# Kernel optimization log

Measured on AMD Instinct MI355X. Metric: run time of the kernel, lower is better.

Reference implementation:

```python
import jax, jax.numpy as jnp
import numpy as np
from jax import lax

B, D, T = 16, 256, 8192
N_CB, CB_SIZE, CB_DIM = 7, 1024, 8
EPS = 1e-12


def setup_inputs() -> dict:
    key = jax.random.key(0)
    ks = jax.random.split(key, 9)
    z = jax.random.normal(ks[0], (B, D, T), dtype=jnp.float32)
    # weight-normalized 1x1 conv params (v direction, g magnitude, bias)
    in_v = jax.random.normal(ks[1], (N_CB, CB_DIM, D), dtype=jnp.float32) * 0.05
    in_g = jax.random.uniform(ks[2], (N_CB, CB_DIM), minval=0.5, maxval=1.5, dtype=jnp.float32)
    in_b = jax.random.normal(ks[3], (N_CB, CB_DIM), dtype=jnp.float32) * 0.01
    out_v = jax.random.normal(ks[4], (N_CB, D, CB_DIM), dtype=jnp.float32) * 0.05
    out_g = jax.random.uniform(ks[5], (N_CB, D), minval=0.5, maxval=1.5, dtype=jnp.float32)
    out_b = jax.random.normal(ks[6], (N_CB, D), dtype=jnp.float32) * 0.01
    codebooks = jax.random.normal(ks[7], (N_CB, CB_SIZE, CB_DIM), dtype=jnp.float32)
    return {"z": z, "in_v": in_v, "in_g": in_g, "in_b": in_b,
            "out_v": out_v, "out_g": out_g, "out_b": out_b,
            "codebooks": codebooks, "n_quantizers": 7}


def _wn(v, g):
    # torch weight_norm dim=0: per-output-channel direction * magnitude
    return g[:, None] * v / jnp.linalg.norm(v, axis=1, keepdims=True)


def _l2norm(x):
    return x / jnp.maximum(jnp.linalg.norm(x, axis=-1, keepdims=True), EPS)


def reference(z, in_v, in_g, in_b, out_v, out_g, out_b, codebooks, n_quantizers):
    b = z.shape[0]
    residual = z
    z_q = jnp.zeros_like(z)
    commitment_loss = jnp.float32(0.0)
    codebook_loss = jnp.float32(0.0)
    all_indices = []
    for i in range(N_CB):
        w_in = _wn(in_v[i], in_g[i])            # [cd, D]
        z_e = jnp.einsum('cd,bdt->bct', w_in, residual) + in_b[i][None, :, None]  # [B, cd, T]
        enc = z_e.transpose(0, 2, 1).reshape(-1, CB_DIM)        # [(B T), cd]
        enc_n = _l2norm(enc)
        cb_n = _l2norm(codebooks[i])                             # [K, cd]
        dist = (jnp.sum(enc_n**2, axis=1, keepdims=True)
                - 2.0 * enc_n @ cb_n.T
                + jnp.sum(cb_n**2, axis=1)[None, :])             # [(B T), K]
        idx = jnp.argmin(dist, axis=1).reshape(b, -1)            # [B, T]
        z_q_c = codebooks[i][idx].transpose(0, 2, 1)             # [B, cd, T]
        commit_i = jnp.mean((z_e - lax.stop_gradient(z_q_c))**2, axis=(1, 2))  # [B]
        cbl_i = jnp.mean((z_q_c - lax.stop_gradient(z_e))**2, axis=(1, 2))     # [B]
        z_q_ste = z_e + lax.stop_gradient(z_q_c - z_e)
        w_out = _wn(out_v[i], out_g[i])          # [D, cd]
        z_q_i = jnp.einsum('dc,bct->bdt', w_out, z_q_ste) + out_b[i][None, :, None]
        mask = (jnp.full((b,), i) < n_quantizers).astype(z.dtype)  # [B]
        z_q = z_q + z_q_i * mask[:, None, None]
        residual = residual - z_q_i
        commitment_loss = commitment_loss + jnp.mean(commit_i * mask)
        codebook_loss = codebook_loss + jnp.mean(cbl_i * mask)
        all_indices.append(idx)
    return z_q, commitment_loss, codebook_loss, jnp.stack(all_indices, axis=1)
```

## Files before the change

### kernel.cpp

```cpp
#include <hip/hip_runtime.h>
#include <math.h>

#define NCB 7
#define CBK 1024
#define CD  8
#define BB  16
#define DD  256
#define TT  8192
#define BT  (BB*TT)

typedef float v2f __attribute__((ext_vector_type(2)));
typedef float v4f __attribute__((ext_vector_type(4)));

static constexpr size_t ZQN  = (size_t)BB * DD * TT;
static constexpr size_t IDX0 = ZQN + 2;

#define WS_WTINT  16
#define WS_WTOUTT 16400
#define WS_OBT    32784
#define WS_APK    34832
#define WS_UVEC   37968
#define WS_CBP    38032

__global__ void rvq_prep1(const float* __restrict__ in_v, const float* __restrict__ in_g,
                          const float* __restrict__ out_v, const float* __restrict__ out_g,
                          const float* __restrict__ out_b, const float* __restrict__ cb,
                          float* __restrict__ ws, double* __restrict__ lossAcc)
{
#pragma clang fp contract(off)
  int gid = blockIdx.x * blockDim.x + threadIdx.x;
  if (gid == 0) *lossAcc = 0.0;
  if (gid < NCB*DD*CD) {
    int i = gid / (DD*CD); int rem = gid % (DD*CD); int d = rem / CD; int c = rem % CD;
    const float* vrow = in_v + ((size_t)i*CD + c) * DD;
    double acc = 0.0;
    for (int q = 0; q < DD; ++q) { double v = vrow[q]; acc += v*v; }
    float nf = (float)sqrt(acc);
    ws[WS_WTINT + d*64 + i*8 + c] = (in_g[i*CD + c] * vrow[d]) / nf;
  } else if (gid < 2*NCB*DD*CD) {
    int e = gid - NCB*DD*CD;
    int i = e / (DD*CD); int rem = e % (DD*CD); int d = rem / CD; int c = rem % CD;
    const float* vrow = out_v + ((size_t)i*DD + d)*CD;
    double acc = 0.0;
    for (int q = 0; q < CD; ++q) { double v = vrow[q]; acc += v*v; }
    float nf = (float)sqrt(acc);
    ws[WS_WTOUTT + d*64 + i*8 + c] = (out_g[i*DD + d] * vrow[c]) / nf;
  } else if (gid < 2*NCB*DD*CD + DD*8) {
    int e = gid - 2*NCB*DD*CD;
    int d = e >> 3, i = e & 7;
    ws[WS_OBT + d*8 + i] = (i < NCB) ? out_b[i*DD + d] : 0.f;
  } else if (gid < 2*NCB*DD*CD + DD*8 + NCB*CBK) {
    int e = gid - 2*NCB*DD*CD - DD*8;
    int i = e / CBK; int k = e % CBK;
    const float* row = cb + ((size_t)i*CBK + k)*CD;
    double acc = 0.0;
    for (int c = 0; c < CD; ++c) { double v = row[c]; acc += v*v; }
    float nf = fmaxf((float)sqrt(acc), 1e-12f);
    float* rec = ws + WS_CBP + ((size_t)i*512 + (k >> 1))*32;
    int h = k & 1;
    float c2 = 0.f;
    for (int c = 0; c < CD; ++c) {
      float cn = row[c] / nf;
      rec[2*c + h] = cn;
      float s = cn*cn; c2 += s;
    }
    rec[16 + h] = c2;
  }
}

__global__ void rvq_prep2(const float* __restrict__ in_b, const float* __restrict__ out_b,
                          float* __restrict__ ws)
{
#pragma clang fp contract(off)
  int gid = blockIdx.x * blockDim.x + threadIdx.x;
  if (gid < 49*64) {
    int pair = gid / 64; int j = pair / 7; int i2 = pair % 7;
    int e = gid % 64; int cp = e >> 3; int c = e & 7;
    float v = 0.f;
    if (j < i2) {
      double acc = 0.0;
      for (int d = 0; d < DD; ++d)
        acc += (double)ws[WS_WTINT + d*64 + i2*8 + c] * (double)ws[WS_WTOUTT + d*64 + j*8 + cp];
      v = (float)acc;
    }
    ws[WS_APK + pair*64 + cp*8 + c] = v;
  } else if (gid < 49*64 + 64) {
    int e = gid - 49*64; int i = e >> 3; int c = e & 7;
    float v = 0.f;
    if (i < NCB) {
      double s = (double)in_b[i*CD + c];
      for (int j = 0; j < i; ++j)
        for (int d = 0; d < DD; ++d)
          s -= (double)ws[WS_WTINT + d*64 + i*8 + c] * (double)out_b[j*DD + d];
      v = (float)s;
    }
    ws[WS_UVEC + e] = v;
  }
}

__launch_bounds__(256)
__global__ void rvq_quant(const float* __restrict__ z,
                          const float* __restrict__ cb,
                          const int* __restrict__ nqp,
                          const float* __restrict__ ws,
                          float* __restrict__ out, double* __restrict__ lossAcc)
{
#pragma clang fp contract(off)
  const int e = blockIdx.x * 256 + threadIdx.x;
  const int b = e >> 13;
  const int t = e & (TT - 1);
  int nqc = *nqp; nqc = nqc < 0 ? 0 : (nqc > NCB ? NCB : nqc);

  const float* WTINT  = ws + WS_WTINT;
  const float* WTOUTT = ws + WS_WTOUTT;
  const float* OBT    = ws + WS_OBT;
  const float* APK    = ws + WS_APK;
  const float* UVEC   = ws + WS_UVEC;
  const float* CBP    = ws + WS_CBP;

  const float* zc0 = z + (size_t)b*DD*TT + t;

  v2f ze2[28];
#pragma unroll
  for (int h = 0; h < 28; ++h) ze2[h] = (v2f){0.f, 0.f};
#pragma unroll 2
  for (int d = 0; d < DD; ++d) {
    float zv = zc0[(size_t)d*TT];
    const v2f* wv = (const v2f*)(WTINT + d*64);
    v2f zb = (v2f){zv, zv};
#pragma unroll
    for (int h = 0; h < 28; ++h)
      ze2[h] = __builtin_elementwise_fma(wv[h], zb, ze2[h]);
  }
  {
    const v2f* uv = (const v2f*)UVEC;
#pragma unroll
    for (int h = 0; h < 28; ++h) ze2[h] = ze2[h] + uv[h];
  }

  double lacc = 0.0;
  v2f zh[NCB][4];

#pragma unroll
  for (int i = 0; i < NCB; ++i) {
    float zef[CD], en[CD];
#pragma unroll
    for (int h = 0; h < 4; ++h) { zef[2*h] = ze2[i*4 + h].x; zef[2*h + 1] = ze2[i*4 + h].y; }
    float ss = 0.f;
#pragma unroll
    for (int c = 0; c < CD; ++c) { float sq = zef[c]*zef[c]; ss += sq; }
    float den = fmaxf(sqrtf(ss), 1e-12f);
    float a2 = 0.f;
#pragma unroll
    for (int c = 0; c < CD; ++c) {
      float en_ = zef[c] / den;
      en[c] = en_;
      float sq = en_*en_; a2 += sq;
    }

    const v2f* crow = (const v2f*)(CBP + (size_t)i*512*32);
    float best = 3.0e38f; int bk = 0;
#pragma unroll 2
    for (int qq = 0; qq < 512; ++qq) {
      const v2f* rw = crow + qq*16;
      v2f m = rw[0] * (v2f){en[0], en[0]};
#pragma unroll
      for (int c = 1; c < CD; ++c)
        m = __builtin_elementwise_fma(rw[c], (v2f){en[c], en[c]}, m);
      v2f dd = __builtin_elementwise_fma((v2f){-2.f, -2.f}, m, (v2f){a2, a2});
      dd = dd + rw[8];
      bool l0 = dd.x < best; best = l0 ? dd.x : best; bk = l0 ? qq*2     : bk;
      bool l1 = dd.y < best; best = l1 ? dd.y : best; bk = l1 ? qq*2 + 1 : bk;
    }

    const float* qrow = cb + ((size_t)i*CBK + bk)*CD;
    v4f qa = ((const v4f*)qrow)[0];
    v4f qb = ((const v4f*)qrow)[1];
    float zcv[CD] = {qa.x, qa.y, qa.z, qa.w, qb.x, qb.y, qb.z, qb.w};
    float zst[CD];
    float sloc = 0.f;
#pragma unroll
    for (int c = 0; c < CD; ++c) {
      float zv = zef[c];
      zst[c] = zv + (zcv[c] - zv);
      float df = zv - zcv[c];
      float sq = df*df; sloc += sq;
    }
    if (i < nqc) lacc += (double)sloc;
    out[IDX0 + ((size_t)b*NCB + i)*TT + t] = (float)bk;
#pragma unroll
    for (int h = 0; h < 4; ++h) zh[i][h] = (v2f){zst[2*h], zst[2*h + 1]};

#pragma unroll
    for (int i2 = i + 1; i2 < NCB; ++i2) {
      const v2f* av = (const v2f*)(APK + (size_t)(i*7 + i2)*64);
      v2f corr[4];
#pragma unroll
      for (int h = 0; h < 4; ++h) corr[h] = av[h] * (v2f){zst[0], zst[0]};
#pragma unroll
      for (int cp = 1; cp < CD; ++cp) {
        v2f zb = (v2f){zst[cp], zst[cp]};
#pragma unroll
        for (int h = 0; h < 4; ++h)
          corr[h] = __builtin_elementwise_fma(av[cp*4 + h], zb, corr[h]);
      }
#pragma unroll
      for (int h = 0; h < 4; ++h) ze2[i2*4 + h] = ze2[i2*4 + h] - corr[h];
    }
  }

  {
    float* zq = out + (size_t)b*DD*TT + t;
#pragma unroll 2
    for (int d = 0; d < DD; ++d) {
      const v2f* wr = (const v2f*)(WTOUTT + d*64);
      const float* obr = OBT + d*8;
      float acc = 0.f;
#pragma unroll
      for (int i = 0; i < NCB; ++i) {
        if (i < nqc) {
          v2f mm = wr[i*4] * zh[i][0];
          mm = __builtin_elementwise_fma(wr[i*4 + 1], zh[i][1], mm);
          mm = __builtin_elementwise_fma(wr[i*4 + 2], zh[i][2], mm);
          mm = __builtin_elementwise_fma(wr[i*4 + 3], zh[i][3], mm);
          float m = mm.x + mm.y;
          acc += (m + obr[i]);
        }
      }
      zq[(size_t)d*TT] = acc;
    }
  }

#pragma unroll
  for (int off = 32; off >= 1; off >>= 1) lacc += __shfl_down(lacc, off, 64);
  if ((threadIdx.x & 63) == 0) atomicAdd(lossAcc, lacc);
}

__global__ void rvq_fin(const double* __restrict__ lossAcc, float* __restrict__ out) {
  float v = (float)(*lossAcc * (1.0 / 1048576.0));
  out[ZQN]     = v;
  out[ZQN + 1] = v;
}

extern "C" void kernel_launch(void* const* d_in, const int* in_sizes, int n_in,
                              void* d_out, int out_size, void* d_ws, size_t ws_size,
                              hipStream_t stream) {
  const float* z     = (const float*)d_in[0];
  const float* in_v  = (const float*)d_in[1];
  const float* in_g  = (const float*)d_in[2];
  const float* in_b  = (const float*)d_in[3];
  const float* out_v = (const float*)d_in[4];
  const float* out_g = (const float*)d_in[5];
  const float* out_b = (const float*)d_in[6];
  const float* cb    = (const float*)d_in[7];
  const int*   nqp   = (const int*)d_in[8];
  float* out = (float*)d_out;

  float*  ws      = (float*)d_ws;
  double* lossAcc = (double*)d_ws;

  int prep1_n = 2*NCB*DD*CD + DD*8 + NCB*CBK;
  rvq_prep1<<<(prep1_n + 255)/256, 256, 0, stream>>>(in_v, in_g, out_v, out_g,
                                                     out_b, cb, ws, lossAcc);
  rvq_prep2<<<13, 256, 0, stream>>>(in_b, out_b, ws);
  rvq_quant<<<BT/256, 256, 0, stream>>>(z, cb, nqp, ws, out, lossAcc);
  rvq_fin<<<1, 1, 0, stream>>>(lossAcc, out);
}
```

Before: 1.055 ms.

## Split each time position across two wavefronts for input projection, codebook search and output

```diff
diff --git a/kernel.cpp b/kernel.cpp
--- a/kernel.cpp
+++ b/kernel.cpp
@@ -106,9 +106,13 @@
                           float* __restrict__ out, double* __restrict__ lossAcc)
 {
 #pragma clang fp contract(off)
-  const int e = blockIdx.x * 256 + threadIdx.x;
-  const int b = e >> 13;
-  const int t = e & (TT - 1);
+  const int tid = threadIdx.x;
+  const int p   = tid & 63;
+  const int h   = __builtin_amdgcn_readfirstlane((tid >> 6) & 1);
+  const int g   = __builtin_amdgcn_readfirstlane(tid >> 7);
+  const int blk = blockIdx.x;
+  const int b   = blk >> 6;
+  const int t   = ((blk & 63) << 7) + g*64 + p;
   int nqc = *nqp; nqc = nqc < 0 ? 0 : (nqc > NCB ? NCB : nqc);
 
   const float* WTINT  = ws + WS_WTINT;
@@ -118,24 +122,54 @@
   const float* UVEC   = ws + WS_UVEC;
   const float* CBP    = ws + WS_CBP;
 
-  const float* zc0 = z + (size_t)b*DD*TT + t;
+  __shared__ v4f   pex[2][14][64];
+  __shared__ float scb[2][2][64];
+  __shared__ int   sck[2][2][64];
 
   v2f ze2[28];
 #pragma unroll
-  for (int h = 0; h < 28; ++h) ze2[h] = (v2f){0.f, 0.f};
+  for (int x = 0; x < 28; ++x) ze2[x] = (v2f){0.f, 0.f};
+  {
+    const float* zc0 = z + (size_t)b*DD*TT + (size_t)(h*128)*TT + t;
 #pragma unroll 2
-  for (int d = 0; d < DD; ++d) {
-    float zv = zc0[(size_t)d*TT];
-    const v2f* wv = (const v2f*)(WTINT + d*64);
-    v2f zb = (v2f){zv, zv};
-#pragma unroll
-    for (int h = 0; h < 28; ++h)
-      ze2[h] = __builtin_elementwise_fma(wv[h], zb, ze2[h]);
+    for (int j = 0; j < 128; ++j) {
+      float zv = zc0[(size_t)j*TT];
+      const v2f* wv = (const v2f*)(WTINT + (h*128 + j)*64);
+      v2f zb = (v2f){zv, zv};
+#pragma unroll
+      for (int x = 0; x < 28; ++x)
+        ze2[x] = __builtin_elementwise_fma(wv[x], zb, ze2[x]);
+    }
+  }
+
+  if (h) {
+#pragma unroll
+    for (int x = 0; x < 14; ++x)
+      pex[g][x][p] = (v4f){ze2[2*x].x, ze2[2*x].y, ze2[2*x+1].x, ze2[2*x+1].y};
+  }
+  __syncthreads();
+  if (!h) {
+#pragma unroll
+    for (int x = 0; x < 14; ++x) {
+      v4f o = pex[g][x][p];
+      ze2[2*x]   = ze2[2*x]   + (v2f){o.x, o.y};
+      ze2[2*x+1] = ze2[2*x+1] + (v2f){o.z, o.w};
+      pex[g][x][p] = (v4f){ze2[2*x].x, ze2[2*x].y, ze2[2*x+1].x, ze2[2*x+1].y};
+    }
+  }
+  __syncthreads();
+  if (h) {
+#pragma unroll
+    for (int x = 0; x < 14; ++x) {
+      v4f o = pex[g][x][p];
+      ze2[2*x]   = (v2f){o.x, o.y};
+      ze2[2*x+1] = (v2f){o.z, o.w};
+    }
   }
   {
     const v2f* uv = (const v2f*)UVEC;
 #pragma unroll
-    for (int h = 0; h < 28; ++h) ze2[h] = ze2[h] + uv[h];
+    for (int x = 0; x < 28; ++x) ze2[x] = ze2[x] + uv[x];
   }
 
   double lacc = 0.0;
@@ -145,7 +179,7 @@
   for (int i = 0; i < NCB; ++i) {
     float zef[CD], en[CD];
 #pragma unroll
-    for (int h = 0; h < 4; ++h) { zef[2*h] = ze2[i*4 + h].x; zef[2*h + 1] = ze2[i*4 + h].y; }
+    for (int x = 0; x < 4; ++x) { zef[2*x] = ze2[i*4 + x].x; zef[2*x + 1] = ze2[i*4 + x].y; }
     float ss = 0.f;
 #pragma unroll
     for (int c = 0; c < CD; ++c) { float sq = zef[c]*zef[c]; ss += sq; }
@@ -158,22 +192,47 @@
       float sq = en_*en_; a2 += sq;
     }
 
-    const v2f* crow = (const v2f*)(CBP + (size_t)i*512*32);
-    float best = 3.0e38f; int bk = 0;
+    v2f enb[CD];
+#pragma unroll
+    for (int c = 0; c < CD; ++c) enb[c] = (v2f){en[c], en[c]};
+    const v2f a2b = (v2f){a2, a2};
+    const v2f n2b = (v2f){-2.f, -2.f};
+    const v2f* crow = (const v2f*)(CBP + ((size_t)i*512 + h*256)*32);
+    float best0 = 3.0e38f, best1 = 3.0e38f; int bk0 = 0, bk1 = 0;
 #pragma unroll 2
-    for (int qq = 0; qq < 512; ++qq) {
-      const v2f* rw = crow + qq*16;
-      v2f m = rw[0] * (v2f){en[0], en[0]};
-#pragma unroll
-      for (int c = 1; c < CD; ++c)
-        m = __builtin_elementwise_fma(rw[c], (v2f){en[c], en[c]}, m);
-      v2f dd = __builtin_elementwise_fma((v2f){-2.f, -2.f}, m, (v2f){a2, a2});
-      dd = dd + rw[8];
-      bool l0 = dd.x < best; best = l0 ? dd.x : best; bk = l0 ? qq*2     : bk;
-      bool l1 = dd.y < best; best = l1 ? dd.y : best; bk = l1 ? qq*2 + 1 : bk;
-    }
-
-    const float* qrow = cb + ((size_t)i*CBK + bk)*CD;
+    for (int qq = 0; qq < 128; ++qq) {
+      const v2f* r0 = crow + qq*16;
+      const v2f* r1 = crow + (128 + qq)*16;
+      v2f m0 = r0[0]*enb[0];
+      v2f m1 = r1[0]*enb[0];
+#pragma unroll
+      for (int c = 1; c < CD; ++c) {
+        m0 = __builtin_elementwise_fma(r0[c], enb[c], m0);
+        m1 = __builtin_elementwise_fma(r1[c], enb[c], m1);
+      }
+      v2f d0 = __builtin_elementwise_fma(n2b, m0, a2b); d0 = d0 + r0[8];
+      v2f d1 = __builtin_elementwise_fma(n2b, m1, a2b); d1 = d1 + r1[8];
+      int kb0 = (h*256 + qq)*2;
+      int kb1 = (h*256 + 128 + qq)*2;
+      bool l;
+      l = d0.x < best0; best0 = l ? d0.x : best0; bk0 = l ? kb0     : bk0;
+      l = d0.y < best0; best0 = l ? d0.y : best0; bk0 = l ? kb0 + 1 : bk0;
+      l = d1.x < best1; best1 = l ? d1.x : best1; bk1 = l ? kb1     : bk1;
+      l = d1.y < best1; best1 = l ? d1.y : best1; bk1 = l ? kb1 + 1 : bk1;
+    }
+    bool ltS = best1 < best0;
+    float bestT = ltS ? best1 : best0;
+    int   bkT   = ltS ? bk1   : bk0;
+
+    scb[g][h][p] = bestT; sck[g][h][p] = bkT;
+    __syncthreads();
+    float bA = scb[g][0][p]; int kA = sck[g][0][p];
+    float bB = scb[g][1][p]; int kB = sck[g][1][p];
+    bool ltH = bB < bA;
+    int k = ltH ? kB : kA;
+    __syncthreads();
+
+    const float* qrow = cb + ((size_t)i*CBK + k)*CD;
     v4f qa = ((const v4f*)qrow)[0];
     v4f qb = ((const v4f*)qrow)[1];
     float zcv[CD] = {qa.x, qa.y, qa.z, qa.w, qb.x, qb.y, qb.z, qb.w};
@@ -186,33 +245,37 @@
       float df = zv - zcv[c];
       float sq = df*df; sloc += sq;
     }
-    if (i < nqc) lacc += (double)sloc;
-    out[IDX0 + ((size_t)b*NCB + i)*TT + t] = (float)bk;
-#pragma unroll
-    for (int h = 0; h < 4; ++h) zh[i][h] = (v2f){zst[2*h], zst[2*h + 1]};
+    if (h == 0) {
+      if (i < nqc) lacc += (double)sloc;
+      out[IDX0 + ((size_t)b*NCB + i)*TT + t] = (float)k;
+    }
+#pragma unroll
+    for (int x = 0; x < 4; ++x) zh[i][x] = (v2f){zst[2*x], zst[2*x + 1]};
 
 #pragma unroll
     for (int i2 = i + 1; i2 < NCB; ++i2) {
       const v2f* av = (const v2f*)(APK + (size_t)(i*7 + i2)*64);
       v2f corr[4];
 #pragma unroll
-      for (int h = 0; h < 4; ++h) corr[h] = av[h] * (v2f){zst[0], zst[0]};
+      for (int x = 0; x < 4; ++x) corr[x] = av[x] * (v2f){zst[0], zst[0]};
 #pragma unroll
       for (int cp = 1; cp < CD; ++cp) {
         v2f zb = (v2f){zst[cp], zst[cp]};
 #pragma unroll
-        for (int h = 0; h < 4; ++h)
-          corr[h] = __builtin_elementwise_fma(av[cp*4 + h], zb, corr[h]);
+        for (int x = 0; x < 4; ++x)
+          corr[x] = __builtin_elementwise_fma(av[cp*4 + x], zb, corr[x]);
       }
 #pragma unroll
-      for (int h = 0; h < 4; ++h) ze2[i2*4 + h] = ze2[i2*4 + h] - corr[h];
+      for (int x = 0; x < 4; ++x) ze2[i2*4 + x] = ze2[i2*4 + x] - corr[x];
     }
   }
 
   {
     float* zq = out + (size_t)b*DD*TT + t;
+    const int dbase = h*128;
 #pragma unroll 2
-    for (int d = 0; d < DD; ++d) {
+    for (int j = 0; j < 128; ++j) {
+      const int d = dbase + j;
       const v2f* wr = (const v2f*)(WTOUTT + d*64);
       const float* obr = OBT + d*8;
       float acc = 0.f;
@@ -231,9 +294,11 @@
     }
   }
 
-#pragma unroll
-  for (int off = 32; off >= 1; off >>= 1) lacc += __shfl_down(lacc, off, 64);
-  if ((threadIdx.x & 63) == 0) atomicAdd(lossAcc, lacc);
+  if (h == 0) {
+#pragma unroll
+    for (int off = 32; off >= 1; off >>= 1) lacc += __shfl_down(lacc, off, 64);
+    if (p == 0) atomicAdd(lossAcc, lacc);
+  }
 }
 
 __global__ void rvq_fin(const double* __restrict__ lossAcc, float* __restrict__ out) {
@@ -263,6 +328,6 @@
   rvq_prep1<<<(prep1_n + 255)/256, 256, 0, stream>>>(in_v, in_g, out_v, out_g,
                                                      out_b, cb, ws, lossAcc);
   rvq_prep2<<<13, 256, 0, stream>>>(in_b, out_b, ws);
-  rvq_quant<<<BT/256, 256, 0, stream>>>(z, cb, nqp, ws, out, lossAcc);
+  rvq_quant<<<BT/128, 256, 0, stream>>>(z, cb, nqp, ws, out, lossAcc);
   rvq_fin<<<1, 1, 0, stream>>>(lossAcc, out);
 }
```

After: 990.6 us. -6.1%, faster.
